# Kernel tuning notes

Hardware: AMD Instinct MI355X
Metric: run time of the kernel (lower is better)

The kernel has to match this reference:

```python
import jax, jax.numpy as jnp
import numpy as np

DIM = 1024
NUM_HEADS = 16
HEAD_DIM = DIM // NUM_HEADS
MLP_HIDDEN = 4 * DIM
SCALE = HEAD_DIM ** -0.5
EPS = 1e-5


def setup_inputs() -> dict:
    key = jax.random.key(0)
    ks = jax.random.split(key, 6)
    s = (2.0 / DIM) ** 0.5
    sd = (2.0 / MLP_HIDDEN) ** 0.5
    return {
        "x": jax.random.normal(ks[0], (2, 2048, DIM), dtype=jnp.float32),
        "attn_qkv_weight": jax.random.normal(ks[1], (3 * DIM, DIM), dtype=jnp.float32) * s,
        "attn_out_weight": jax.random.normal(ks[2], (DIM, DIM), dtype=jnp.float32) * s,
        "norm1_weight": jnp.ones((DIM,), jnp.float32),
        "norm1_bias": jnp.zeros((DIM,), jnp.float32),
        "mlp_gate_weight": jax.random.normal(ks[3], (MLP_HIDDEN, DIM), dtype=jnp.float32) * s,
        "mlp_up_weight": jax.random.normal(ks[4], (MLP_HIDDEN, DIM), dtype=jnp.float32) * s,
        "mlp_down_weight": jax.random.normal(ks[5], (DIM, MLP_HIDDEN), dtype=jnp.float32) * sd,
        "norm2_weight": jnp.ones((DIM,), jnp.float32),
        "norm2_bias": jnp.zeros((DIM,), jnp.float32),
    }


def _layer_norm(x, w, b):
    mean = x.mean(axis=-1, keepdims=True)
    var = jnp.mean(jnp.square(x - mean), axis=-1, keepdims=True)
    return (x - mean) / jnp.sqrt(var + EPS) * w + b


def reference(x, attn_qkv_weight, attn_out_weight, norm1_weight, norm1_bias,
              mlp_gate_weight, mlp_up_weight, mlp_down_weight, norm2_weight, norm2_bias):
    B, S, D = x.shape
    residual1 = x
    xn = _layer_norm(x, norm1_weight, norm1_bias)
    qkv = xn @ attn_qkv_weight.T                      # [B,S,3D]
    qkv = qkv.reshape(B, S, 3, NUM_HEADS, HEAD_DIM).transpose(2, 0, 3, 1, 4)
    q, k, v = qkv[0], qkv[1], qkv[2]                  # [B,H,S,hd]
    scores = jnp.einsum('bhqd,bhkd->bhqk', q, k) * SCALE  # full O(S^2) matrix
    attn = jax.nn.softmax(scores, axis=-1)            # no causal mask (default False)
    out = jnp.einsum('bhqk,bhkd->bhqd', attn, v)      # [B,H,S,hd]
    out = out.transpose(0, 2, 1, 3).reshape(B, S, D)
    x2 = residual1 + out @ attn_out_weight.T
    xn2 = _layer_norm(x2, norm2_weight, norm2_bias)
    gate = xn2 @ mlp_gate_weight.T
    up = xn2 @ mlp_up_weight.T
    hidden = jax.nn.silu(gate) * up
    return x2 + hidden @ mlp_down_weight.T
```

## Files before the change

### kernel.cpp

```cpp
#include <hip/hip_runtime.h>

typedef float f32x4 __attribute__((ext_vector_type(4)));
typedef __bf16 bf16x8 __attribute__((ext_vector_type(8)));
typedef unsigned int u32;

#define DEV __device__ __forceinline__
#define WAITVM(n) asm volatile("s_waitcnt vmcnt(" #n ")" ::: "memory")

DEV void gload_lds16(const void* g, void* l) {
  __builtin_amdgcn_global_load_lds(
      (const __attribute__((address_space(1))) u32*)g,
      (__attribute__((address_space(3))) u32*)l, 16, 0, 0);
}

DEV int xcd_swz(int flat, int nwg) {
  return (flat & 7) * (nwg >> 3) + (flat >> 3);
}

__global__ __launch_bounds__(256) void cvt_bf16(const float* __restrict__ in,
                                                __bf16* __restrict__ o, int n) {
  int i = (blockIdx.x * 256 + threadIdx.x) * 8;
  if (i >= n) return;
  float4 a = *(const float4*)(in + i);
  float4 b = *(const float4*)(in + i + 4);
  union { bf16x8 v; __bf16 e[8]; } u;
  u.e[0] = (__bf16)a.x; u.e[1] = (__bf16)a.y; u.e[2] = (__bf16)a.z; u.e[3] = (__bf16)a.w;
  u.e[4] = (__bf16)b.x; u.e[5] = (__bf16)b.y; u.e[6] = (__bf16)b.z; u.e[7] = (__bf16)b.w;
  *(bf16x8*)(o + i) = u.v;
}

__global__ __launch_bounds__(256) void ln_kernel(const float* __restrict__ x,
                                                 const float* __restrict__ w,
                                                 const float* __restrict__ b,
                                                 __bf16* __restrict__ o) {
  const int row = blockIdx.x, tid = threadIdx.x;
  const float4 v = ((const float4*)(x + (size_t)row * 1024))[tid];
  float s  = v.x + v.y + v.z + v.w;
  float s2 = v.x * v.x + v.y * v.y + v.z * v.z + v.w * v.w;
  for (int off = 32; off; off >>= 1) {
    s  += __shfl_down(s, off);
    s2 += __shfl_down(s2, off);
  }
  __shared__ float rs[4], rs2[4];
  if ((tid & 63) == 0) { rs[tid >> 6] = s; rs2[tid >> 6] = s2; }
  __syncthreads();
  float S = rs[0] + rs[1] + rs[2] + rs[3];
  float S2 = rs2[0] + rs2[1] + rs2[2] + rs2[3];
  float mean = S * (1.0f / 1024.0f);
  float var = S2 * (1.0f / 1024.0f) - mean * mean;
  float inv = rsqrtf(var + 1e-5f);
  const float4 wv = ((const float4*)w)[tid];
  const float4 bv = ((const float4*)b)[tid];
  union { ushort4 u4; __bf16 e[4]; } u;
  u.e[0] = (__bf16)((v.x - mean) * inv * wv.x + bv.x);
  u.e[1] = (__bf16)((v.y - mean) * inv * wv.y + bv.y);
  u.e[2] = (__bf16)((v.z - mean) * inv * wv.z + bv.z);
  u.e[3] = (__bf16)((v.w - mean) * inv * wv.w + bv.w);
  *(ushort4*)(o + (size_t)row * 1024 + tid * 4) = u.u4;
}


template <int EPI, int MI>
__global__ __launch_bounds__(256) void gemm_bt(const __bf16* __restrict__ A,
                                               const __bf16* __restrict__ B,
                                               void* __restrict__ Cout,
                                               const float* __restrict__ Res,
                                               int M, int N, int K) {
  constexpr int BM = MI * 32;
  __shared__ __align__(16) __bf16 As[3][BM * 32];
  __shared__ __align__(16) __bf16 Bs[3][128 * 32];
  const int tid = threadIdx.x;
  const int lane = tid & 63;
  const int w = tid >> 6;
  const int wr = w >> 1, wc = w & 1;
  const int l15 = lane & 15, g = lane >> 4;
  const int c8 = ((g + (l15 >> 1)) & 3) * 8;

  const int nbx = gridDim.x;
  const int logical = xcd_swz(blockIdx.y * nbx + blockIdx.x, nbx * gridDim.y);
  const int bm = (logical / nbx) * BM, bn = (logical % nbx) * 128;

  f32x4 acc[MI][4] = {};

  auto stage = [&](int buf, int k0) {
#pragma unroll
    for (int p = 0; p < MI / 2; ++p) {
      const int ch = p * 256 + tid;
      const int row = ch >> 2;
      const int gc = ((ch & 3) - ((ch >> 3) & 3)) & 3;
      gload_lds16(A + (size_t)(bm + row) * K + k0 + gc * 8,
                  &As[buf][(p * 256 + w * 64) * 8]);
    }
#pragma unroll
    for (int p = 0; p < 2; ++p) {
      const int ch = p * 256 + tid;
      const int row = ch >> 2;
      const int gc = ((ch & 3) - ((ch >> 3) & 3)) & 3;
      gload_lds16(B + (size_t)(bn + row) * K + k0 + gc * 8,
                  &Bs[buf][(p * 256 + w * 64) * 8]);
    }
  };

  const int NT = K >> 5;
  stage(0, 0);
  stage(1, 32);

  int cur = 0;
  for (int t = 0; t < NT; ++t) {
    if (t + 1 < NT) {
      if constexpr (MI == 4) { WAITVM(4); } else { WAITVM(3); }
    } else {
      WAITVM(0);
    }
    __builtin_amdgcn_s_barrier();
    if (t + 2 < NT) {
      int sb = cur + 2; if (sb >= 3) sb -= 3;
      stage(sb, (t + 2) * 32);
    }
    bf16x8 af[MI], bfr[4];
#pragma unroll
    for (int i = 0; i < MI; ++i)
      af[i] = *(const bf16x8*)(&As[cur][(wr * (MI * 16) + i * 16 + l15) * 32 + c8]);
#pragma unroll
    for (int j = 0; j < 4; ++j)
      bfr[j] = *(const bf16x8*)(&Bs[cur][(wc * 64 + j * 16 + l15) * 32 + c8]);
#pragma unroll
    for (int i = 0; i < MI; ++i)
#pragma unroll
      for (int j = 0; j < 4; ++j)
        acc[i][j] = __builtin_amdgcn_mfma_f32_16x16x32_bf16(af[i], bfr[j], acc[i][j], 0, 0, 0);
    cur = (cur == 2) ? 0 : cur + 1;
  }

  const int r0 = bm + wr * (MI * 16) + g * 4;
  const int c0 = bn + wc * 64 + l15;
#pragma unroll
  for (int i = 0; i < MI; ++i)
#pragma unroll
    for (int j = 0; j < 4; ++j)
#pragma unroll
      for (int r = 0; r < 4; ++r) {
        const size_t idx = (size_t)(r0 + i * 16 + r) * N + (c0 + j * 16);
        const float v = acc[i][j][r];
        if (EPI == 0) ((__bf16*)Cout)[idx] = (__bf16)v;
        else          ((float*)Cout)[idx] = v + Res[idx];
      }
}

__global__ __launch_bounds__(256, 2) void gemm_mlp(const __bf16* __restrict__ A,
                                                   const __bf16* __restrict__ BG,
                                                   const __bf16* __restrict__ BU,
                                                   __bf16* __restrict__ H,
                                                   int M, int N, int K) {
  __shared__ __align__(16) __bf16 As[3][128 * 32];
  __shared__ __align__(16) __bf16 Bg[3][128 * 32];
  __shared__ __align__(16) __bf16 Bu[3][128 * 32];
  const int tid = threadIdx.x;
  const int lane = tid & 63;
  const int w = tid >> 6;
  const int wr = w >> 1, wc = w & 1;
  const int l15 = lane & 15, g = lane >> 4;
  const int c8 = ((g + (l15 >> 1)) & 3) * 8;

  const int nbx = gridDim.x;
  const int logical = xcd_swz(blockIdx.y * nbx + blockIdx.x, nbx * gridDim.y);
  const int bm = (logical / nbx) * 128, bn = (logical % nbx) * 128;

  f32x4 accg[4][4] = {};
  f32x4 accu[4][4] = {};

  auto stage = [&](int buf, int k0) {
#pragma unroll
    for (int p = 0; p < 2; ++p) {
      const int ch = p * 256 + tid;
      const int row = ch >> 2;
      const int gc = ((ch & 3) - ((ch >> 3) & 3)) & 3;
      const int coff = gc * 8;
      const int dst = (p * 256 + w * 64) * 8;
      gload_lds16(A + (size_t)(bm + row) * K + k0 + coff, &As[buf][dst]);
      gload_lds16(BG + (size_t)(bn + row) * K + k0 + coff, &Bg[buf][dst]);
      gload_lds16(BU + (size_t)(bn + row) * K + k0 + coff, &Bu[buf][dst]);
    }
  };

  const int NT = K >> 5;
  stage(0, 0);
  stage(1, 32);

  int cur = 0;
  for (int t = 0; t < NT; ++t) {
    if (t + 1 < NT) { WAITVM(6); } else { WAITVM(0); }
    __builtin_amdgcn_s_barrier();
    if (t + 2 < NT) {
      int sb = cur + 2; if (sb >= 3) sb -= 3;
      stage(sb, (t + 2) * 32);
    }
    bf16x8 af[4], bgf[4], buf_[4];
#pragma unroll
    for (int i = 0; i < 4; ++i)
      af[i] = *(const bf16x8*)(&As[cur][(wr * 64 + i * 16 + l15) * 32 + c8]);
#pragma unroll
    for (int j = 0; j < 4; ++j) {
      bgf[j] = *(const bf16x8*)(&Bg[cur][(wc * 64 + j * 16 + l15) * 32 + c8]);
      buf_[j] = *(const bf16x8*)(&Bu[cur][(wc * 64 + j * 16 + l15) * 32 + c8]);
    }
#pragma unroll
    for (int i = 0; i < 4; ++i)
#pragma unroll
      for (int j = 0; j < 4; ++j) {
        accg[i][j] = __builtin_amdgcn_mfma_f32_16x16x32_bf16(af[i], bgf[j], accg[i][j], 0, 0, 0);
        accu[i][j] = __builtin_amdgcn_mfma_f32_16x16x32_bf16(af[i], buf_[j], accu[i][j], 0, 0, 0);
      }
    cur = (cur == 2) ? 0 : cur + 1;
  }

  const int r0 = bm + wr * 64 + g * 4;
  const int c0 = bn + wc * 64 + l15;
#pragma unroll
  for (int i = 0; i < 4; ++i)
#pragma unroll
    for (int j = 0; j < 4; ++j)
#pragma unroll
      for (int r = 0; r < 4; ++r) {
        const float gt = accg[i][j][r];
        const float ut = accu[i][j][r];
        const float h = gt / (1.0f + __expf(-gt)) * ut;
        H[(size_t)(r0 + i * 16 + r) * N + (c0 + j * 16)] = (__bf16)h;
      }
}

__global__ __launch_bounds__(256) void transpose_v(const __bf16* __restrict__ qkv,
                                                   __bf16* __restrict__ vT) {
  const int st = blockIdx.x, bh = blockIdx.y;
  const int b = bh >> 4, h = bh & 15;
  __shared__ __bf16 tile[64][80];
  const int tid = threadIdx.x;
#pragma unroll
  for (int it = 0; it < 2; ++it) {
    const int idx = it * 256 + tid;
    const int r = idx >> 3, c0 = (idx & 7) * 8;
    bf16x8 v = *(const bf16x8*)(qkv + (size_t)(b * 2048 + st * 64 + r) * 3072 + 2048 + h * 64 + c0);
    *(bf16x8*)&tile[r][c0] = v;
  }
  __syncthreads();
#pragma unroll
  for (int it = 0; it < 2; ++it) {
    const int idx = it * 256 + tid;
    const int d = idx >> 3, s0 = (idx & 7) * 8;
    union { bf16x8 v; __bf16 e[8]; } u;
#pragma unroll
    for (int j = 0; j < 8; ++j) u.e[j] = tile[s0 + j][d];
    *(bf16x8*)(vT + (size_t)(bh * 64 + d) * 2048 + st * 64 + s0) = u.v;
  }
}

__global__ __launch_bounds__(256) void attn_kernel(const __bf16* __restrict__ qkv,
                                                   const __bf16* __restrict__ vT,
                                                   __bf16* __restrict__ outp) {
  const int logical = xcd_swz(blockIdx.y * 32 + blockIdx.x, 1024);
  const int qt = logical & 31, bh = logical >> 5;
  const int b = bh >> 4, h = bh & 15;
  const int tid = threadIdx.x, lane = tid & 63, w = tid >> 6;
  const int l15 = lane & 15, g = lane >> 4;
  const float CSC = 0.125f * 1.44269504f;

  __shared__ __align__(16) __bf16 Ks[64 * 64];
  __shared__ __align__(16) __bf16 Vs[64 * 64];
  __shared__ __align__(16) __bf16 Ps[4][16 * 80];

  const int qrow = qt * 64 + w * 16 + l15;
  const size_t qbase = (size_t)(b * 2048 + qrow) * 3072 + h * 64;
  const bf16x8 qf0 = *(const bf16x8*)(qkv + qbase + g * 8);
  const bf16x8 qf1 = *(const bf16x8*)(qkv + qbase + 32 + g * 8);

  f32x4 o_acc[4] = {};
  float l_r[4] = {0.f, 0.f, 0.f, 0.f};

  const size_t kgbase = (size_t)(b * 2048) * 3072 + 1024 + h * 64;
  const size_t vgbase = (size_t)bh * 64 * 2048;

  for (int t = 0; t < 32; ++t) {
    const int kv0 = t * 64;
#pragma unroll
    for (int p = 0; p < 2; ++p) {
      const int ch = p * 256 + w * 64 + lane;
      const int row = ch >> 3, c = ch & 7;
      const int gc = c ^ (row & 7);
      gload_lds16(qkv + kgbase + (size_t)(kv0 + row) * 3072 + gc * 8, Ks + (p * 256 + w * 64) * 8);
      gload_lds16(vT + vgbase + (size_t)row * 2048 + kv0 + gc * 8, Vs + (p * 256 + w * 64) * 8);
    }
    WAITVM(0);
    __syncthreads();

    f32x4 sf[4];
    __builtin_amdgcn_s_setprio(1);
#pragma unroll
    for (int ni = 0; ni < 4; ++ni) {
      const int krow = ni * 16 + l15;
      const __bf16* kb = Ks + krow * 64;
      const bf16x8 kf0 = *(const bf16x8*)(kb + ((g ^ (krow & 7)) * 8));
      const bf16x8 kf1 = *(const bf16x8*)(kb + (((4 + g) ^ (krow & 7)) * 8));
      f32x4 z = {0.f, 0.f, 0.f, 0.f};
      z = __builtin_amdgcn_mfma_f32_16x16x32_bf16(qf0, kf0, z, 0, 0, 0);
      z = __builtin_amdgcn_mfma_f32_16x16x32_bf16(qf1, kf1, z, 0, 0, 0);
      sf[ni] = z;
    }
    __builtin_amdgcn_s_setprio(0);

#pragma unroll
    for (int ni = 0; ni < 4; ++ni)
#pragma unroll
      for (int r = 0; r < 4; ++r) {
        const float pv = exp2f(sf[ni][r] * CSC);
        sf[ni][r] = pv;
        l_r[r] += pv;
      }

    __bf16* pw = Ps[w];
#pragma unroll
    for (int ni = 0; ni < 4; ++ni)
#pragma unroll
      for (int r = 0; r < 4; ++r) {
        const int row = g * 4 + r;
        const int pc = (ni * 2 + (l15 >> 3)) ^ (row & 7);
        pw[row * 80 + pc * 8 + (l15 & 7)] = (__bf16)sf[ni][r];
      }
    asm volatile("" ::: "memory");
    const bf16x8 pa0 = *(const bf16x8*)(pw + l15 * 80 + ((g ^ (l15 & 7)) * 8));
    const bf16x8 pa1 = *(const bf16x8*)(pw + l15 * 80 + (((4 + g) ^ (l15 & 7)) * 8));

    __builtin_amdgcn_s_setprio(1);
#pragma unroll
    for (int ni = 0; ni < 4; ++ni) {
      const int vrow = ni * 16 + l15;
      const __bf16* vb = Vs + vrow * 64;
      const bf16x8 vf0 = *(const bf16x8*)(vb + ((g ^ (vrow & 7)) * 8));
      const bf16x8 vf1 = *(const bf16x8*)(vb + (((4 + g) ^ (vrow & 7)) * 8));
      o_acc[ni] = __builtin_amdgcn_mfma_f32_16x16x32_bf16(pa0, vf0, o_acc[ni], 0, 0, 0);
      o_acc[ni] = __builtin_amdgcn_mfma_f32_16x16x32_bf16(pa1, vf1, o_acc[ni], 0, 0, 0);
    }
    __builtin_amdgcn_s_setprio(0);
    __syncthreads();
  }

#pragma unroll
  for (int mk = 1; mk < 16; mk <<= 1)
#pragma unroll
    for (int r = 0; r < 4; ++r) l_r[r] += __shfl_xor(l_r[r], mk);
#pragma unroll
  for (int r = 0; r < 4; ++r) {
    const int orow = qt * 64 + w * 16 + g * 4 + r;
    const float invl = 1.0f / l_r[r];
#pragma unroll
    for (int ni = 0; ni < 4; ++ni)
      outp[(size_t)(b * 2048 + orow) * 1024 + h * 64 + ni * 16 + l15] =
          (__bf16)(o_acc[ni][r] * invl);
  }
}

extern "C" void kernel_launch(void* const* d_in, const int* in_sizes, int n_in,
                              void* d_out, int out_size, void* d_ws, size_t ws_size,
                              hipStream_t stream) {
  const float* x     = (const float*)d_in[0];
  const float* Wqkv  = (const float*)d_in[1];
  const float* Wout  = (const float*)d_in[2];
  const float* n1w   = (const float*)d_in[3];
  const float* n1b   = (const float*)d_in[4];
  const float* Wgate = (const float*)d_in[5];
  const float* Wup   = (const float*)d_in[6];
  const float* Wdown = (const float*)d_in[7];
  const float* n2w   = (const float*)d_in[8];
  const float* n2b   = (const float*)d_in[9];
  float* out = (float*)d_out;
  char* ws = (char*)d_ws;
  const size_t MB = 1u << 20;

  __bf16* XN  = (__bf16*)(ws + 0);
  __bf16* QKV = (__bf16*)(ws + 8 * MB);
  __bf16* VT  = (__bf16*)(ws + 32 * MB);
  __bf16* ATT = (__bf16*)(ws + 40 * MB);
  float*  X2  = (float*)(ws + 48 * MB);
  __bf16* H   = QKV;
  __bf16* WQ  = (__bf16*)(ws + 64 * MB);
  __bf16* WO  = (__bf16*)(ws + 70 * MB);
  __bf16* WG  = (__bf16*)(ws + 72 * MB);
  __bf16* WU  = (__bf16*)(ws + 80 * MB);
  __bf16* WD  = (__bf16*)(ws + 88 * MB);

  cvt_bf16<<<3145728 / 2048, 256, 0, stream>>>(Wqkv, WQ, 3145728);
  cvt_bf16<<<1048576 / 2048, 256, 0, stream>>>(Wout, WO, 1048576);
  cvt_bf16<<<4194304 / 2048, 256, 0, stream>>>(Wgate, WG, 4194304);
  cvt_bf16<<<4194304 / 2048, 256, 0, stream>>>(Wup, WU, 4194304);
  cvt_bf16<<<4194304 / 2048, 256, 0, stream>>>(Wdown, WD, 4194304);

  ln_kernel<<<4096, 256, 0, stream>>>(x, n1w, n1b, XN);
  gemm_bt<0, 4><<<dim3(24, 32), 256, 0, stream>>>(XN, WQ, QKV, nullptr, 4096, 3072, 1024);
  transpose_v<<<dim3(32, 32), 256, 0, stream>>>(QKV, VT);
  attn_kernel<<<dim3(32, 32), 256, 0, stream>>>(QKV, VT, ATT);
  gemm_bt<1, 2><<<dim3(8, 64), 256, 0, stream>>>(ATT, WO, X2, x, 4096, 1024, 1024);
  ln_kernel<<<4096, 256, 0, stream>>>(X2, n2w, n2b, XN);
  gemm_mlp<<<dim3(32, 32), 256, 0, stream>>>(XN, WG, WU, H, 4096, 4096, 1024);
  gemm_bt<1, 2><<<dim3(8, 64), 256, 0, stream>>>(H, WD, out, X2, 4096, 1024, 4096);

  (void)in_sizes; (void)n_in; (void)out_size; (void)ws_size;
}
```

Before: 312.0 us.

## Load K/V directly from global in attention and group GEMM tile raster

The attention kernel drops the LDS staging of K and V tiles and the per-iteration barriers. Each wave now reads its K and V fragments straight from global memory. The GEMM kernels remap block indices so groups of 8 M-tiles share an N-tile, to improve L2 reuse. The attention change removes synchronization but makes each wave fetch the same K/V data redundantly, relying on caches and exposing global load latency directly in front of the MFMAs.

```diff
diff --git a/kernel.cpp b/kernel.cpp
--- a/kernel.cpp
+++ b/kernel.cpp
@@ -78,7 +78,9 @@
 
   const int nbx = gridDim.x;
   const int logical = xcd_swz(blockIdx.y * nbx + blockIdx.x, nbx * gridDim.y);
-  const int bm = (logical / nbx) * BM, bn = (logical % nbx) * 128;
+  const int per = 8 * nbx, grp = logical / per, rem = logical % per;
+  const int bm = (grp * 8 + (rem & 7)) * BM;
+  const int bn = (rem >> 3) * 128;
 
   f32x4 acc[MI][4] = {};
 
@@ -164,7 +166,9 @@
 
   const int nbx = gridDim.x;
   const int logical = xcd_swz(blockIdx.y * nbx + blockIdx.x, nbx * gridDim.y);
-  const int bm = (logical / nbx) * 128, bn = (logical % nbx) * 128;
+  const int per = 8 * nbx, grp = logical / per, rem = logical % per;
+  const int bm = (grp * 8 + (rem & 7)) * 128;
+  const int bn = (rem >> 3) * 128;
 
   f32x4 accg[4][4] = {};
   f32x4 accu[4][4] = {};
@@ -264,8 +268,6 @@
   const int l15 = lane & 15, g = lane >> 4;
   const float CSC = 0.125f * 1.44269504f;
 
-  __shared__ __align__(16) __bf16 Ks[64 * 64];
-  __shared__ __align__(16) __bf16 Vs[64 * 64];
   __shared__ __align__(16) __bf16 Ps[4][16 * 80];
 
   const int qrow = qt * 64 + w * 16 + l15;
@@ -276,30 +278,19 @@
   f32x4 o_acc[4] = {};
   float l_r[4] = {0.f, 0.f, 0.f, 0.f};
 
-  const size_t kgbase = (size_t)(b * 2048) * 3072 + 1024 + h * 64;
-  const size_t vgbase = (size_t)bh * 64 * 2048;
+  const __bf16* Kb = qkv + (size_t)(b * 2048) * 3072 + 1024 + h * 64;
+  const __bf16* Vb = vT + (size_t)bh * 64 * 2048;
 
   for (int t = 0; t < 32; ++t) {
     const int kv0 = t * 64;
-#pragma unroll
-    for (int p = 0; p < 2; ++p) {
-      const int ch = p * 256 + w * 64 + lane;
-      const int row = ch >> 3, c = ch & 7;
-      const int gc = c ^ (row & 7);
-      gload_lds16(qkv + kgbase + (size_t)(kv0 + row) * 3072 + gc * 8, Ks + (p * 256 + w * 64) * 8);
-      gload_lds16(vT + vgbase + (size_t)row * 2048 + kv0 + gc * 8, Vs + (p * 256 + w * 64) * 8);
-    }
-    WAITVM(0);
-    __syncthreads();
 
     f32x4 sf[4];
     __builtin_amdgcn_s_setprio(1);
 #pragma unroll
     for (int ni = 0; ni < 4; ++ni) {
-      const int krow = ni * 16 + l15;
-      const __bf16* kb = Ks + krow * 64;
-      const bf16x8 kf0 = *(const bf16x8*)(kb + ((g ^ (krow & 7)) * 8));
-      const bf16x8 kf1 = *(const bf16x8*)(kb + (((4 + g) ^ (krow & 7)) * 8));
+      const __bf16* kr = Kb + (size_t)(kv0 + ni * 16 + l15) * 3072;
+      const bf16x8 kf0 = *(const bf16x8*)(kr + g * 8);
+      const bf16x8 kf1 = *(const bf16x8*)(kr + 32 + g * 8);
       f32x4 z = {0.f, 0.f, 0.f, 0.f};
       z = __builtin_amdgcn_mfma_f32_16x16x32_bf16(qf0, kf0, z, 0, 0, 0);
       z = __builtin_amdgcn_mfma_f32_16x16x32_bf16(qf1, kf1, z, 0, 0, 0);
@@ -332,15 +323,13 @@
     __builtin_amdgcn_s_setprio(1);
 #pragma unroll
     for (int ni = 0; ni < 4; ++ni) {
-      const int vrow = ni * 16 + l15;
-      const __bf16* vb = Vs + vrow * 64;
-      const bf16x8 vf0 = *(const bf16x8*)(vb + ((g ^ (vrow & 7)) * 8));
-      const bf16x8 vf1 = *(const bf16x8*)(vb + (((4 + g) ^ (vrow & 7)) * 8));
+      const __bf16* vr = Vb + (size_t)(ni * 16 + l15) * 2048 + kv0;
+      const bf16x8 vf0 = *(const bf16x8*)(vr + g * 8);
+      const bf16x8 vf1 = *(const bf16x8*)(vr + 32 + g * 8);
       o_acc[ni] = __builtin_amdgcn_mfma_f32_16x16x32_bf16(pa0, vf0, o_acc[ni], 0, 0, 0);
       o_acc[ni] = __builtin_amdgcn_mfma_f32_16x16x32_bf16(pa1, vf1, o_acc[ni], 0, 0, 0);
     }
     __builtin_amdgcn_s_setprio(0);
-    __syncthreads();
   }
 
 #pragma unroll
```

Result: slower. 464.7 us (+48.9%).
